# Optimization experiments

Measured on AMD Instinct MI355X. Metric: run time of the kernel, lower is better.

The kernel has to match this reference:

```python
import jax, jax.numpy as jnp
import numpy as np

B, N, D, H_IMG, W_IMG = 1, 6, 128, 28, 60
HB, WB = 50, 50
HEADS, DH = 4, 32
INNER = HEADS * DH  # 128 == D
Q = HB * WB
NK = N * H_IMG * W_IMG


def _ln(x, w, b, eps=1e-5):
    m = jnp.mean(x, axis=-1, keepdims=True)
    v = jnp.var(x, axis=-1, keepdims=True)
    return (x - m) * jax.lax.rsqrt(v + eps) * w + b


def setup_inputs() -> dict:
    key = jax.random.key(0)
    ks = jax.random.split(key, 20)
    s = 0.02
    inp = {
        "q": jax.random.normal(ks[0], (B, D, HB, WB), jnp.float32),
        "k": jax.random.normal(ks[1], (B, N, D, H_IMG, W_IMG), jnp.float32),
        "v": jax.random.normal(ks[2], (B, N, D, H_IMG, W_IMG), jnp.float32),
        "W_logits": jax.random.uniform(ks[3], (B, Q, NK), jnp.float32),
        "vis_flat": jax.random.randint(ks[4], (B, Q, NK), 0, 2).astype(jnp.int32),
        "skip": jax.random.normal(ks[5], (B, D, HB, WB), jnp.float32),
        # LayerNorm params
        "qn_w": jnp.ones((D,), jnp.float32), "qn_b": jnp.zeros((D,), jnp.float32),
        "kn_w": jnp.ones((D,), jnp.float32), "kn_b": jnp.zeros((D,), jnp.float32),
        "vn_w": jnp.ones((D,), jnp.float32), "vn_b": jnp.zeros((D,), jnp.float32),
        "pre_w": jnp.ones((D,), jnp.float32), "pre_b": jnp.zeros((D,), jnp.float32),
        "post_w": jnp.ones((D,), jnp.float32), "post_b": jnp.zeros((D,), jnp.float32),
        # Linear params, stored [in, out]
        "wq": jax.random.normal(ks[6], (D, INNER), jnp.float32) * s,
        "bq": jnp.zeros((INNER,), jnp.float32),
        "wk": jax.random.normal(ks[7], (D, INNER), jnp.float32) * s,
        "bk": jnp.zeros((INNER,), jnp.float32),
        "wv": jax.random.normal(ks[8], (D, INNER), jnp.float32) * s,
        "bv": jnp.zeros((INNER,), jnp.float32),
        "wp": jax.random.normal(ks[9], (INNER, D), jnp.float32) * s,
        "bp": jnp.zeros((D,), jnp.float32),
        "w1": jax.random.normal(ks[10], (D, 2 * D), jnp.float32) * s,
        "b1": jnp.zeros((2 * D,), jnp.float32),
        "w2": jax.random.normal(ks[11], (2 * D, D), jnp.float32) * s,
        "b2": jnp.zeros((D,), jnp.float32),
    }
    return inp


def reference(q, k, v, W_logits, vis_flat, skip,
              qn_w, qn_b, kn_w, kn_b, vn_w, vn_b, pre_w, pre_b, post_w, post_b,
              wq, bq, wk, bk, wv, bv, wp, bp, w1, b1, w2, b2):
    b, d, Hb, Wb = q.shape
    _, n, _, hi, wi = k.shape
    Qn = Hb * Wb
    # b d H W -> b (H W) d ; b n d h w -> b (n h w) d
    qf = q.reshape(b, d, Qn).transpose(0, 2, 1)
    kf = k.transpose(0, 1, 3, 4, 2).reshape(b, n * hi * wi, d)
    vf = v.transpose(0, 1, 3, 4, 2).reshape(b, n * hi * wi, d)
    qf = _ln(qf, qn_w, qn_b)
    kf = _ln(kf, kn_w, kn_b)
    vf = _ln(vf, vn_w, vn_b)
    qh = (qf @ wq + bq).reshape(b, Qn, HEADS, DH).transpose(0, 2, 1, 3)
    kh = (kf @ wk + bk).reshape(b, -1, HEADS, DH).transpose(0, 2, 1, 3)
    vh = (vf @ wv + bv).reshape(b, -1, HEADS, DH).transpose(0, 2, 1, 3)
    scale = DH ** (-0.5)
    logits = jnp.einsum('bhqd,bhkd->bhqk', qh, kh) * scale  # [b,h,Q,NK]
    neg_inf = jnp.finfo(logits.dtype).min
    logits = jnp.where(vis_flat[:, None] == 0, neg_inf, logits)
    logits = logits * W_logits[:, None]  # multiplicative EAF weighting
    attn = jax.nn.softmax(logits, axis=-1)
    out = jnp.einsum('bhqk,bhkd->bhqd', attn, vh)
    out = out.transpose(0, 2, 1, 3).reshape(b, Qn, INNER)
    out = out @ wp + bp
    z = out + skip.reshape(b, d, Qn).transpose(0, 2, 1)
    z = _ln(z, pre_w, pre_b)
    z = z + (jax.nn.gelu(z @ w1 + b1, approximate=False) @ w2 + b2)
    z = _ln(z, post_w, post_b)
    return z.transpose(0, 2, 1).reshape(b, d, Hb, Wb)
```

## Files before the change

### kernel.cpp

```cpp
#include <hip/hip_runtime.h>
#include <hip/hip_bf16.h>
#include <math.h>

typedef short short8 __attribute__((ext_vector_type(8)));
typedef float floatx4 __attribute__((ext_vector_type(4)));
typedef int   intx4  __attribute__((ext_vector_type(4)));

#define D 128
#define Q 2500
#define QPAD 2560
#define NK 10080
#define NKPAD 10112
#define SPLITS 19
#define CPS 17
#define OPS 163904
#define LPS 10304
#define VBW 320
#define VROW 40
#define QSCALE 0.25501268426834347f
#define NEGBIG -3.0e38f

#define LDS_BARRIER() asm volatile("s_waitcnt lgkmcnt(0)\n\ts_barrier" ::: "memory")

__device__ __forceinline__ unsigned short f2bf(float f) {
    unsigned u = __float_as_uint(f);
    unsigned r = (u + 0x7fffu + ((u >> 16) & 1u)) >> 16;
    return (unsigned short)r;
}
__device__ __forceinline__ unsigned pack2bf(float lo, float hi) {
    unsigned u0 = __float_as_uint(lo) + 0x8000u;
    unsigned u1 = __float_as_uint(hi) + 0x8000u;
    return (u0 >> 16) | (u1 & 0xffff0000u);
}
__device__ __forceinline__ unsigned cvtpk(float lo, float hi) {
    unsigned r;
    asm("v_cvt_pk_bf16_f32 %0, %1, %2" : "=v"(r) : "v"(lo), "v"(hi));
    return r;
}
__device__ __forceinline__ float bflo(unsigned u) { return __uint_as_float(u << 16); }
__device__ __forceinline__ float bfhi(unsigned u) { return __uint_as_float(u & 0xffff0000u); }

__global__ __launch_bounds__(256) void prep_kernel(
    const float* __restrict__ qi, const float* __restrict__ ki, const float* __restrict__ vi,
    const float* __restrict__ qw, const float* __restrict__ qb_,
    const float* __restrict__ kw, const float* __restrict__ kb,
    const float* __restrict__ vw, const float* __restrict__ vb,
    unsigned short* __restrict__ xq, unsigned short* __restrict__ xk,
    unsigned short* __restrict__ xv,
    const float* __restrict__ wq, const float* __restrict__ wk,
    const float* __restrict__ wv, const float* __restrict__ wp,
    const float* __restrict__ w1, const float* __restrict__ w2,
    unsigned short* __restrict__ wqT, unsigned short* __restrict__ wkT,
    unsigned short* __restrict__ wvT, unsigned short* __restrict__ wpT,
    unsigned short* __restrict__ w1T, unsigned short* __restrict__ w2T,
    const int* __restrict__ vis, unsigned* __restrict__ vbits) {
    int bid = blockIdx.x, t = threadIdx.x;
    if (bid >= 1227) {
        int row = bid - 1227;
        const int* src = vis + (size_t)row * NK;
        #pragma unroll 2
        for (int w = t; w < 315; w += 256) {
            unsigned bits = 0;
            const intx4* p = (const intx4*)(src + w * 32);
            #pragma unroll
            for (int g = 0; g < 8; g++) {
                intx4 v = p[g];
                #pragma unroll
                for (int j = 0; j < 4; j++) bits |= (v[j] ? 1u : 0u) << (g * 4 + j);
            }
            vbits[(size_t)row * VBW + w] = bits;
        }
        return;
    }
    if (bid >= 715) {
        int idx = (bid - 715) * 256 + t;
        if (idx < 49152) {
            int m = idx >> 14;
            int local = idx & 16383;
            int n = local >> 7, kk = local & 127;
            const float* w = (m == 0) ? wq : ((m == 1) ? wk : wv);
            unsigned short* o = (m == 0) ? wqT : ((m == 1) ? wkT : wvT);
            o[local] = f2bf(w[kk * 128 + n]);
        } else if (idx < 65536) {
            int local = idx - 49152;
            int n = local >> 7, kk = local & 127;
            wpT[local] = f2bf(wp[kk * 128 + n]);
        } else if (idx < 98304) {
            int local = idx - 65536;
            int n = local >> 7, kk = local & 127;
            w1T[local] = f2bf(w1[kk * 256 + n]);
        } else {
            int local = idx - 98304;
            int n = local >> 8, kk = local & 255;
            w2T[local] = f2bf(w2[kk * 128 + n]);
        }
        return;
    }
    __shared__ float lds2[32 * 132];
    const float* src; unsigned short* dst; const float *g, *b;
    int S, valid;
    if (bid < 79) {
        int p0 = bid * 32;
        src = qi + p0; S = Q; dst = xq + p0 * D; g = qw; b = qb_;
        valid = Q - p0; if (valid > 32) valid = 32;
    } else if (bid < 397) {
        int tt = bid - 79;
        int n = tt / 53, tile = tt - n * 53, r = tile * 32;
        src = ki + (size_t)(n * 128) * 1680 + r; S = 1680;
        dst = xk + (n * 1680 + r) * D; g = kw; b = kb;
        valid = 1680 - r; if (valid > 32) valid = 32;
    } else {
        int tt = bid - 397;
        int n = tt / 53, tile = tt - n * 53, r = tile * 32;
        src = vi + (size_t)(n * 128) * 1680 + r; S = 1680;
        dst = xv + (n * 1680 + r) * D; g = vw; b = vb;
        valid = 1680 - r; if (valid > 32) valid = 32;
    }
    #pragma unroll
    for (int pass = 0; pass < 4; pass++) {
        int s = pass * 256 + t;
        int d = s >> 3, ps = s & 7;
        floatx4 val = {0.f, 0.f, 0.f, 0.f};
        if (ps * 4 < valid) val = *(const floatx4*)(src + (size_t)d * S + ps * 4);
        #pragma unroll
        for (int j = 0; j < 4; j++) lds2[(ps * 4 + j) * 132 + d] = val[j];
    }
    __syncthreads();
    int lane = t & 63, wvx = t >> 6;
    int pos = wvx * 8 + (lane >> 3), l7 = lane & 7;
    floatx4 x4[4];
    #pragma unroll
    for (int k = 0; k < 4; k++) x4[k] = *(const floatx4*)(&lds2[pos * 132 + l7 * 16 + k * 4]);
    float s = 0.f, ss = 0.f;
    #pragma unroll
    for (int k = 0; k < 4; k++)
        #pragma unroll
        for (int j = 0; j < 4; j++) { s += x4[k][j]; ss += x4[k][j] * x4[k][j]; }
    #pragma unroll
    for (int m = 1; m <= 4; m <<= 1) { s += __shfl_xor(s, m, 64); ss += __shfl_xor(ss, m, 64); }
    float mean = s * (1.0f / 128.0f);
    float var = ss * (1.0f / 128.0f) - mean * mean;
    float rstd = rsqrtf(var + 1e-5f);
    short8 o1, o2;
    #pragma unroll
    for (int k = 0; k < 4; k++) {
        floatx4 g4 = *(const floatx4*)(g + l7 * 16 + k * 4);
        floatx4 b4 = *(const floatx4*)(b + l7 * 16 + k * 4);
        #pragma unroll
        for (int j = 0; j < 4; j++) {
            float o = (x4[k][j] - mean) * rstd * g4[j] + b4[j];
            if (k < 2) o1[k * 4 + j] = (short)f2bf(o);
            else o2[(k - 2) * 4 + j] = (short)f2bf(o);
        }
    }
    if (pos < valid) {
        *(short8*)(dst + pos * D + l7 * 16) = o1;
        *(short8*)(dst + pos * D + l7 * 16 + 8) = o2;
    }
}

__global__ __launch_bounds__(256) void proj_kernel(
    const unsigned short* __restrict__ xq, const unsigned short* __restrict__ xk,
    const unsigned short* __restrict__ xv,
    const unsigned short* __restrict__ wqT, const unsigned short* __restrict__ wkT,
    const unsigned short* __restrict__ wvT,
    const float* __restrict__ bq, const float* __restrict__ bk, const float* __restrict__ bv,
    unsigned short* __restrict__ qh, unsigned short* __restrict__ kh,
    unsigned short* __restrict__ vhT) {
    __shared__ short vlds[128 * 72];
    int bid = blockIdx.x;
    const unsigned short *src, *wT; const float* bias; int mb, mode; float scale;
    if (bid < 40)       { mode = 0; src = xq; wT = wqT; bias = bq; mb = bid * 64; scale = QSCALE; }
    else if (bid < 198) { mode = 1; src = xk; wT = wkT; bias = bk; mb = (bid - 40) * 64; scale = 1.0f; }
    else                { mode = 2; src = xv; wT = wvT; bias = bv; mb = (bid - 198) * 64; scale = 1.0f; }
    int t = threadIdx.x, wave = t >> 6, lane = t & 63;
    int l15 = lane & 15, quad = lane >> 4;
    int m0 = mb + wave * 16;
    floatx4 acc[8];
    #pragma unroll
    for (int i = 0; i < 8; i++) acc[i] = (floatx4){0.f, 0.f, 0.f, 0.f};
    #pragma unroll
    for (int kf = 0; kf < 4; kf++) {
        short8 A = *(const short8*)(src + (m0 + l15) * D + kf * 32 + quad * 8);
        #pragma unroll
        for (int nt = 0; nt < 8; nt++) {
            short8 Bv = *(const short8*)(wT + (nt * 16 + l15) * D + kf * 32 + quad * 8);
            acc[nt] = __builtin_amdgcn_mfma_f32_16x16x32_bf16(A, Bv, acc[nt], 0, 0, 0);
        }
    }
    if (mode != 2) {
        unsigned short* dst = (mode == 0) ? qh : kh;
        #pragma unroll
        for (int nt = 0; nt < 8; nt++) {
            float bb = bias[nt * 16 + l15];
            #pragma unroll
            for (int r = 0; r < 4; r++)
                dst[(m0 + quad * 4 + r) * D + nt * 16 + l15] = f2bf((acc[nt][r] + bb) * scale);
        }
    } else {
        #pragma unroll
        for (int nt = 0; nt < 8; nt++) {
            float bb = bias[nt * 16 + l15];
            #pragma unroll
            for (int r = 0; r < 4; r++)
                vlds[(nt * 16 + l15) * 72 + (wave * 16 + quad * 4 + r)] =
                    (short)f2bf(acc[nt][r] + bb);
        }
        __syncthreads();
        int pr = t & 31, dd = t >> 5;
        int sub = pr >> 4, i = pr & 15;
        #pragma unroll
        for (int pass = 0; pass < 16; pass++) {
            int d = pass * 8 + dd;
            unsigned lo = (unsigned short)vlds[d * 72 + sub * 32 + i];
            unsigned hi = (unsigned short)vlds[d * 72 + sub * 32 + 16 + i];
            *(unsigned*)(vhT + (size_t)d * NKPAD + mb + sub * 32 + 2 * i) = lo | (hi << 16);
        }
    }
}

template<int USEBITS>
__global__ __launch_bounds__(256, 3) void attn_kernel_t(
    const unsigned short* __restrict__ qh, const unsigned short* __restrict__ kh,
    const unsigned short* __restrict__ vhT,
    const float* __restrict__ Wl, const int* __restrict__ vis,
    const unsigned* __restrict__ vbits,
    unsigned* __restrict__ OpartU, float* __restrict__ lpart) {
    __shared__ short Kl[2][32 * 136];
    __shared__ short Vl[2][128 * VROW];
    int bid = blockIdx.x;
    int split = bid % SPLITS, qt = bid / SPLITS;
    int t = threadIdx.x, wave = t >> 6, lane = t & 63;
    int l15 = lane & 15, quad = lane >> 4;
    int qb = qt * 64 + wave * 16;
    int k00 = split * (CPS * 32);
    int cmax = (NK - k00) >> 5; if (cmax > CPS) cmax = CPS;

    short8 qB[4];
    #pragma unroll
    for (int h = 0; h < 4; h++)
        qB[h] = *(const short8*)(qh + (size_t)(qb + l15) * D + h * 32 + quad * 8);

    int kr = t >> 3, ks = (t & 7) * 2;
    int vd = t >> 1, vs = (t & 1) * 2;
    const uint4* ksrc = (const uint4*)(kh + (size_t)(k00 + kr) * D + ks * 8);
    const uint4* vsrc = (const uint4*)(vhT + (size_t)vd * NKPAD + k00 + vs * 8);
    short* kdst = &Kl[0][kr * 136 + ks * 8];
    short* vdst = &Vl[0][vd * VROW + vs * 8];

    int wrow = qb + l15; if (wrow >= Q) wrow = Q - 1;
    const float* wp = Wl + (size_t)wrow * NK + k00 + quad * 4;
    const int*   vp = vis + (size_t)wrow * NK + k00 + quad * 4;
    const unsigned* vbp = vbits + (size_t)wrow * VBW + split * CPS;

    int idxA = l15 + ((quad & 1) << 5);
    int idxB = idxA + 16;
    bool hiK = (quad >= 2);

    const floatx4 zf = {0.f, 0.f, 0.f, 0.f};
    floatx4 O[4][2];
    float lacc[4];
    #pragma unroll
    for (int h = 0; h < 4; h++) { O[h][0] = zf; O[h][1] = zf; lacc[h] = 0.f; }

    uint4 ka = ksrc[0], kb2 = ksrc[1];
    uint4 va = vsrc[0], vb2 = vsrc[1];
    floatx4 wc0 = *(const floatx4*)wp;
    floatx4 wc1 = *(const floatx4*)(wp + 16);
    floatx4 wn0, wn1;
    intx4 vc0, vc1;
    unsigned vbc = 0, vbn = 0;
    if constexpr (USEBITS) {
        vbc = vbp[0];
        wn0 = *(const floatx4*)(wp + 32);
        wn1 = *(const floatx4*)(wp + 48);
        vbn = vbp[1];
    } else {
        vc0 = *(const intx4*)vp;
        vc1 = *(const intx4*)(vp + 16);
    }
    *(uint4*)kdst = ka;       *(uint4*)(kdst + 8) = kb2;
    *(uint4*)vdst = va;       *(uint4*)(vdst + 8) = vb2;

    #pragma unroll 1
    for (int c = 0; c < cmax; c++) {
        LDS_BARRIER();
        int buf = c & 1;
        uint4 nka, nkb, nva, nvb;
        floatx4 w20, w21; intx4 vn0, vn1;
        unsigned vb2n = 0;
        if (c + 1 < cmax) {
            const uint4* ks2 = ksrc + (size_t)(c + 1) * 512;
            const uint4* vs2 = vsrc + (size_t)(c + 1) * 4;
            nka = ks2[0]; nkb = ks2[1];
            nva = vs2[0]; nvb = vs2[1];
        }
        if constexpr (USEBITS) {
            if (c + 2 < cmax) {
                w20 = *(const floatx4*)(wp + (c + 2) * 32);
                w21 = *(const floatx4*)(wp + (c + 2) * 32 + 16);
                vb2n = vbp[c + 2];
            }
        } else {
            if (c + 1 < cmax) {
                wn0 = *(const floatx4*)(wp + (c + 1) * 32);
                wn1 = *(const floatx4*)(wp + (c + 1) * 32 + 16);
                vn0 = *(const intx4*)(vp + (c + 1) * 32);
                vn1 = *(const intx4*)(vp + (c + 1) * 32 + 16);
            }
        }
        float a2[8], b2[8];
        if constexpr (USEBITS) {
            unsigned bq = vbc >> (quad * 4);
            #pragma unroll
            for (int r = 0; r < 4; r++) {
                bool m0 = (bq >> r) & 1u;
                bool m1 = (bq >> (16 + r)) & 1u;
                a2[r]     = m0 ? wc0[r] : 0.f;
                b2[r]     = m0 ? 0.f : wc0[r] * NEGBIG;
                a2[4 + r] = m1 ? wc1[r] : 0.f;
                b2[4 + r] = m1 ? 0.f : wc1[r] * NEGBIG;
            }
        } else {
            #pragma unroll
            for (int r = 0; r < 4; r++) {
                a2[r]     = vc0[r] ? wc0[r] : 0.f;
                b2[r]     = vc0[r] ? 0.f : wc0[r] * NEGBIG;
                a2[4 + r] = vc1[r] ? wc1[r] : 0.f;
                b2[4 + r] = vc1[r] ? 0.f : wc1[r] * NEGBIG;
            }
        }
        const short* Kb = Kl[buf];
        const short* Vb = Vl[buf];
        __builtin_amdgcn_s_setprio(1);
        #pragma unroll
        for (int h = 0; h < 4; h++) {
            short8 kA0 = *(const short8*)(Kb + l15 * 136 + h * 32 + quad * 8);
            short8 kA1 = *(const short8*)(Kb + (16 + l15) * 136 + h * 32 + quad * 8);
            floatx4 S0 = __builtin_amdgcn_mfma_f32_16x16x32_bf16(kA0, qB[h], zf, 0, 0, 0);
            floatx4 S1 = __builtin_amdgcn_mfma_f32_16x16x32_bf16(kA1, qB[h], zf, 0, 0, 0);
            float p0[4], p1[4];
            #pragma unroll
            for (int r = 0; r < 4; r++) {
                p0[r] = exp2f(S0[r] * a2[r] + b2[r]);
                p1[r] = exp2f(S1[r] * a2[4 + r] + b2[4 + r]);
                lacc[h] += p0[r] + p1[r];
            }
            unsigned u0 = cvtpk(p0[0], p0[1]);
            unsigned u1 = cvtpk(p0[2], p0[3]);
            unsigned u2 = cvtpk(p1[0], p1[1]);
            unsigned u3 = cvtpk(p1[2], p1[3]);
            unsigned s0A = __shfl(u0, idxA, 64), s2A = __shfl(u2, idxA, 64);
            unsigned s1A = __shfl(u1, idxA, 64), s3A = __shfl(u3, idxA, 64);
            unsigned s0B = __shfl(u0, idxB, 64), s2B = __shfl(u2, idxB, 64);
            unsigned s1B = __shfl(u1, idxB, 64), s3B = __shfl(u3, idxB, 64);
            union { unsigned u[4]; short8 s8; } pb;
            pb.u[0] = hiK ? s2A : s0A;
            pb.u[1] = hiK ? s3A : s1A;
            pb.u[2] = hiK ? s2B : s0B;
            pb.u[3] = hiK ? s3B : s1B;
            short8 vA0 = *(const short8*)(Vb + (h * 32 + l15) * VROW + quad * 8);
            short8 vA1 = *(const short8*)(Vb + (h * 32 + 16 + l15) * VROW + quad * 8);
            O[h][0] = __builtin_amdgcn_mfma_f32_16x16x32_bf16(vA0, pb.s8, O[h][0], 0, 0, 0);
            O[h][1] = __builtin_amdgcn_mfma_f32_16x16x32_bf16(vA1, pb.s8, O[h][1], 0, 0, 0);
        }
        __builtin_amdgcn_s_setprio(0);
        if (c + 1 < cmax) {
            short* kd = buf ? kdst : (kdst + 32 * 136);
            short* vd2 = buf ? vdst : (vdst + 128 * VROW);
            *(uint4*)kd = nka;       *(uint4*)(kd + 8) = nkb;
            *(uint4*)vd2 = nva;      *(uint4*)(vd2 + 8) = nvb;
        }
        if constexpr (USEBITS) {
            wc0 = wn0; wc1 = wn1; vbc = vbn;
            if (c + 2 < cmax) { wn0 = w20; wn1 = w21; vbn = vb2n; }
        } else {
            if (c + 1 < cmax) { wc0 = wn0; wc1 = wn1; vc0 = vn0; vc1 = vn1; }
        }
    }

    int row = qb + l15;
    #pragma unroll
    for (int h = 0; h < 4; h++) {
        float lv = lacc[h];
        lv += __shfl_xor(lv, 16, 64);
        lv += __shfl_xor(lv, 32, 64);
        if (quad == 0) lpart[(size_t)split * LPS + row * 4 + h] = lv;
        #pragma unroll
        for (int tl = 0; tl < 2; tl++) {
            uint2 o2;
            o2.x = cvtpk(O[h][tl][0], O[h][tl][1]);
            o2.y = cvtpk(O[h][tl][2], O[h][tl][3]);
            *(uint2*)(OpartU + (size_t)split * OPS + ((size_t)row * 4 + h) * 16 + tl * 8 + quad * 2) = o2;
        }
    }
}

__global__ __launch_bounds__(128) void combine_kernel(
    const unsigned* __restrict__ Opart, const float* __restrict__ lpart,
    unsigned* __restrict__ A1u) {
    int tid = blockIdx.x * 128 + threadIdx.x;
    int sl = tid & 3, he = (tid >> 2) & 3, grow = tid >> 4;
    float lsum = 0.f;
    #pragma unroll 5
    for (int sp = 0; sp < SPLITS; sp++) lsum += lpart[(size_t)sp * LPS + grow * 4 + he];
    float inv = 1.0f / fmaxf(lsum, 1e-30f);
    size_t base = ((size_t)grow * 4 + he) * 16 + sl * 4;
    float a0 = 0.f, a1 = 0.f, a2 = 0.f, a3 = 0.f, a4 = 0.f, a5 = 0.f, a6 = 0.f, a7 = 0.f;
    #pragma unroll 5
    for (int sp = 0; sp < SPLITS; sp++) {
        uint4 u = *(const uint4*)(Opart + (size_t)sp * OPS + base);
        a0 += bflo(u.x); a1 += bfhi(u.x);
        a2 += bflo(u.y); a3 += bfhi(u.y);
        a4 += bflo(u.z); a5 += bfhi(u.z);
        a6 += bflo(u.w); a7 += bfhi(u.w);
    }
    uint4 o;
    o.x = pack2bf(a0 * inv, a1 * inv);
    o.y = pack2bf(a2 * inv, a3 * inv);
    o.z = pack2bf(a4 * inv, a5 * inv);
    o.w = pack2bf(a6 * inv, a7 * inv);
    *(uint4*)(A1u + (size_t)grow * 64 + he * 16 + sl * 4) = o;
}

__global__ __launch_bounds__(256) void mlp_kernel(
    const unsigned short* __restrict__ A1,
    const unsigned short* __restrict__ wpT,
    const float* __restrict__ bp, const float* __restrict__ skip,
    const float* __restrict__ pre_w, const float* __restrict__ pre_b,
    const unsigned short* __restrict__ w1T, const float* __restrict__ b1,
    const unsigned short* __restrict__ w2T, const float* __restrict__ b2,
    const float* __restrict__ post_w, const float* __restrict__ post_b,
    float* __restrict__ out) {
    __shared__ __align__(16) char smem[51200];
    short* Z1 = (short*)smem;
    short* H1 = (short*)(smem + 17408);
    float* Zout = (float*)smem;

    int qb = blockIdx.x * 64;
    int t = threadIdx.x, wave = t >> 6, lane = t & 63;
    int l15 = lane & 15, quad = lane >> 4;
    int m0 = wave * 16;

    floatx4 z[8];
    #pragma unroll
    for (int i = 0; i < 8; i++) z[i] = (floatx4){0.f, 0.f, 0.f, 0.f};
    #pragma unroll
    for (int kf = 0; kf < 4; kf++) {
        short8 A = *(const short8*)(A1 + (size_t)(qb + m0 + l15) * 128 + kf * 32 + quad * 8);
        #pragma unroll
        for (int nt = 0; nt < 8; nt++) {
            short8 Bv = *(const short8*)(wpT + (nt * 16 + l15) * D + kf * 32 + quad * 8);
            z[nt] = __builtin_amdgcn_mfma_f32_16x16x32_bf16(A, Bv, z[nt], 0, 0, 0);
        }
    }
    float Zv[8][4];
    #pragma unroll
    for (int nt = 0; nt < 8; nt++) {
        int n = nt * 16 + l15;
        float bb = bp[n];
        #pragma unroll
        for (int r = 0; r < 4; r++) {
            int q = qb + m0 + quad * 4 + r;
            int qc = q < Q ? q : (Q - 1);
            Zv[nt][r] = z[nt][r] + bb + skip[n * Q + qc];
        }
    }
    float Zn[8][4];
    {
        #pragma unroll
        for (int r = 0; r < 4; r++) {
            float s1 = 0.f, s2 = 0.f;
            #pragma unroll
            for (int nt = 0; nt < 8; nt++) { s1 += Zv[nt][r]; s2 += Zv[nt][r] * Zv[nt][r]; }
            #pragma unroll
            for (int m = 1; m <= 8; m <<= 1) { s1 += __shfl_xor(s1, m, 64); s2 += __shfl_xor(s2, m, 64); }
            float mean = s1 * (1.0f / 128.0f);
            float var = s2 * (1.0f / 128.0f) - mean * mean;
            float rstd = rsqrtf(var + 1e-5f);
            #pragma unroll
            for (int nt = 0; nt < 8; nt++) Zn[nt][r] = (Zv[nt][r] - mean) * rstd;
        }
        #pragma unroll
        for (int nt = 0; nt < 8; nt++) {
            int n = nt * 16 + l15;
            float g = pre_w[n], be = pre_b[n];
            #pragma unroll
            for (int r = 0; r < 4; r++) {
                Zn[nt][r] = Zn[nt][r] * g + be;
                Z1[(m0 + quad * 4 + r) * 136 + n] = (short)f2bf(Zn[nt][r]);
            }
        }
    }
    {
        floatx4 h2[16];
        #pragma unroll
        for (int i = 0; i < 16; i++) h2[i] = (floatx4){0.f, 0.f, 0.f, 0.f};
        #pragma unroll
        for (int kf = 0; kf < 4; kf++) {
            short8 A = *(const short8*)(Z1 + (m0 + l15) * 136 + kf * 32 + quad * 8);
            #pragma unroll
            for (int nt = 0; nt < 16; nt++) {
                short8 Bv = *(const short8*)(w1T + (nt * 16 + l15) * D + kf * 32 + quad * 8);
                h2[nt] = __builtin_amdgcn_mfma_f32_16x16x32_bf16(A, Bv, h2[nt], 0, 0, 0);
            }
        }
        #pragma unroll
        for (int nt = 0; nt < 16; nt++) {
            int n = nt * 16 + l15;
            float bb = b1[n];
            #pragma unroll
            for (int r = 0; r < 4; r++) {
                float x = h2[nt][r] + bb;
                float gl = 0.5f * x * (1.0f + erff(x * 0.70710678118654752f));
                H1[(m0 + quad * 4 + r) * 264 + n] = (short)f2bf(gl);
            }
        }
    }
    floatx4 o3[8];
    #pragma unroll
    for (int i = 0; i < 8; i++) o3[i] = (floatx4){0.f, 0.f, 0.f, 0.f};
    #pragma unroll
    for (int kf = 0; kf < 8; kf++) {
        short8 A = *(const short8*)(H1 + (m0 + l15) * 264 + kf * 32 + quad * 8);
        #pragma unroll
        for (int nt = 0; nt < 8; nt++) {
            short8 Bv = *(const short8*)(w2T + (nt * 16 + l15) * 256 + kf * 32 + quad * 8);
            o3[nt] = __builtin_amdgcn_mfma_f32_16x16x32_bf16(A, Bv, o3[nt], 0, 0, 0);
        }
    }
    float Z2[8][4];
    #pragma unroll
    for (int nt = 0; nt < 8; nt++) {
        int n = nt * 16 + l15;
        float bb = b2[n];
        #pragma unroll
        for (int r = 0; r < 4; r++) Z2[nt][r] = Zn[nt][r] + o3[nt][r] + bb;
    }
    float Zo[8][4];
    {
        #pragma unroll
        for (int r = 0; r < 4; r++) {
            float s1 = 0.f, s2 = 0.f;
            #pragma unroll
            for (int nt = 0; nt < 8; nt++) { s1 += Z2[nt][r]; s2 += Z2[nt][r] * Z2[nt][r]; }
            #pragma unroll
            for (int m = 1; m <= 8; m <<= 1) { s1 += __shfl_xor(s1, m, 64); s2 += __shfl_xor(s2, m, 64); }
            float mean = s1 * (1.0f / 128.0f);
            float var = s2 * (1.0f / 128.0f) - mean * mean;
            float rstd = rsqrtf(var + 1e-5f);
            #pragma unroll
            for (int nt = 0; nt < 8; nt++) Zo[nt][r] = (Z2[nt][r] - mean) * rstd;
        }
        #pragma unroll
        for (int nt = 0; nt < 8; nt++) {
            int n = nt * 16 + l15;
            float g = post_w[n], be = post_b[n];
            #pragma unroll
            for (int r = 0; r < 4; r++) Zo[nt][r] = Zo[nt][r] * g + be;
        }
    }
    __syncthreads();
    #pragma unroll
    for (int nt = 0; nt < 8; nt++)
        #pragma unroll
        for (int r = 0; r < 4; r++)
            Zout[(nt * 16 + l15) * 65 + m0 + quad * 4 + r] = Zo[nt][r];
    __syncthreads();
    {
        int pl = t & 63;
        int q = qb + pl;
        if (q < Q) {
            #pragma unroll
            for (int it = 0; it < 32; it++) {
                int n = it * 4 + (t >> 6);
                out[n * Q + q] = Zout[n * 65 + pl];
            }
        }
    }
}

extern "C" void kernel_launch(void* const* d_in, const int* in_sizes, int n_in,
                              void* d_out, int out_size, void* d_ws, size_t ws_size,
                              hipStream_t stream) {
    (void)in_sizes; (void)n_in; (void)out_size;
    const float* q      = (const float*)d_in[0];
    const float* k      = (const float*)d_in[1];
    const float* v      = (const float*)d_in[2];
    const float* Wl     = (const float*)d_in[3];
    const int*   vis    = (const int*)  d_in[4];
    const float* skip   = (const float*)d_in[5];
    const float* qn_w   = (const float*)d_in[6];
    const float* qn_b   = (const float*)d_in[7];
    const float* kn_w   = (const float*)d_in[8];
    const float* kn_b   = (const float*)d_in[9];
    const float* vn_w   = (const float*)d_in[10];
    const float* vn_b   = (const float*)d_in[11];
    const float* pre_w  = (const float*)d_in[12];
    const float* pre_b  = (const float*)d_in[13];
    const float* post_w = (const float*)d_in[14];
    const float* post_b = (const float*)d_in[15];
    const float* wq     = (const float*)d_in[16];
    const float* bq     = (const float*)d_in[17];
    const float* wk     = (const float*)d_in[18];
    const float* bk     = (const float*)d_in[19];
    const float* wv     = (const float*)d_in[20];
    const float* bv     = (const float*)d_in[21];
    const float* wp     = (const float*)d_in[22];
    const float* bp     = (const float*)d_in[23];
    const float* w1     = (const float*)d_in[24];
    const float* b1     = (const float*)d_in[25];
    const float* w2     = (const float*)d_in[26];
    const float* b2     = (const float*)d_in[27];
    float* out = (float*)d_out;

    char* ws = (char*)d_ws;
    unsigned short* xq  = (unsigned short*)(ws + 0);
    unsigned short* xk  = (unsigned short*)(ws + 655360);
    unsigned short* xv  = (unsigned short*)(ws + 3244032);
    unsigned short* qh  = (unsigned short*)(ws + 5832704);
    unsigned short* kh  = (unsigned short*)(ws + 6488064);
    unsigned short* vhT = (unsigned short*)(ws + 9076736);
    unsigned short* wqT = (unsigned short*)(ws + 11665408);
    unsigned short* wkT = (unsigned short*)(ws + 11698176);
    unsigned short* wvT = (unsigned short*)(ws + 11730944);
    unsigned short* wpT = (unsigned short*)(ws + 11763712);
    unsigned short* w1T = (unsigned short*)(ws + 11796480);
    unsigned short* w2T = (unsigned short*)(ws + 11862016);
    unsigned* OpartU    = (unsigned*)(ws + 11927552);
    float* lpart        = (float*)(ws + 34874112);
    unsigned* vbits     = (unsigned*)(ws + 36316672);
    unsigned* A1u       = (unsigned*)(ws + 0);

    const bool usebits = (ws_size == 0) || (ws_size >= 39520000ull);

    prep_kernel<<<dim3(usebits ? 3727 : 1227), dim3(256), 0, stream>>>(
        q, k, v, qn_w, qn_b, kn_w, kn_b, vn_w, vn_b, xq, xk, xv,
        wq, wk, wv, wp, w1, w2, wqT, wkT, wvT, wpT, w1T, w2T, vis, vbits);
    proj_kernel<<<dim3(356), dim3(256), 0, stream>>>(xq, xk, xv, wqT, wkT, wvT, bq, bk, bv,
                                                     qh, kh, vhT);
    if (usebits)
        attn_kernel_t<1><<<dim3(40 * SPLITS), dim3(256), 0, stream>>>(
            qh, kh, vhT, Wl, vis, vbits, OpartU, lpart);
    else
        attn_kernel_t<0><<<dim3(40 * SPLITS), dim3(256), 0, stream>>>(
            qh, kh, vhT, Wl, vis, vbits, OpartU, lpart);
    combine_kernel<<<dim3(320), dim3(128), 0, stream>>>(OpartU, lpart, A1u);
    mlp_kernel<<<dim3(40), dim3(256), 0, stream>>>((const unsigned short*)A1u, wpT, bp, skip,
                                                   pre_w, pre_b, w1T, b1, w2T, b2,
                                                   post_w, post_b, out);
}
```

Before: 358.5 us.

## Process two 64-row query tiles per attention block to reuse staged K/V tiles

Each attention block now covers 128 query rows instead of 64. Every wave runs two 16-row query sub-tiles against the same K/V chunk in LDS, so each K/V load from global memory and LDS read feeds twice as many MFMAs. To keep the grid large, the key dimension is split into 25 chunks of 13 instead of 19 of 17. The LDS row padding for K and V changes, launch bounds drop to 2 blocks per CU, and the W/visibility prefetch depth for the bitmask path goes from two chunks ahead to one. The cost is higher register pressure and lower occupancy, plus more partial outputs for the combine step to reduce.

```diff
diff --git a/kernel.cpp b/kernel.cpp
--- a/kernel.cpp
+++ b/kernel.cpp
@@ -11,12 +11,13 @@
 #define QPAD 2560
 #define NK 10080
 #define NKPAD 10112
-#define SPLITS 19
-#define CPS 17
+#define SPLITS 25
+#define CPS 13
 #define OPS 163904
 #define LPS 10304
 #define VBW 320
-#define VROW 40
+#define KROW 152
+#define VROW 48
 #define QSCALE 0.25501268426834347f
 #define NEGBIG -3.0e38f
 
@@ -220,64 +221,69 @@
 }
 
 template<int USEBITS>
-__global__ __launch_bounds__(256, 3) void attn_kernel_t(
+__global__ __launch_bounds__(256, 2) void attn_kernel_t(
     const unsigned short* __restrict__ qh, const unsigned short* __restrict__ kh,
     const unsigned short* __restrict__ vhT,
     const float* __restrict__ Wl, const int* __restrict__ vis,
     const unsigned* __restrict__ vbits,
     unsigned* __restrict__ OpartU, float* __restrict__ lpart) {
-    __shared__ short Kl[2][32 * 136];
+    __shared__ short Kl[2][32 * KROW];
     __shared__ short Vl[2][128 * VROW];
     int bid = blockIdx.x;
     int split = bid % SPLITS, qt = bid / SPLITS;
     int t = threadIdx.x, wave = t >> 6, lane = t & 63;
     int l15 = lane & 15, quad = lane >> 4;
-    int qb = qt * 64 + wave * 16;
+    int qb = qt * 128 + wave * 16;
     int k00 = split * (CPS * 32);
     int cmax = (NK - k00) >> 5; if (cmax > CPS) cmax = CPS;
 
-    short8 qB[4];
-    #pragma unroll
-    for (int h = 0; h < 4; h++)
-        qB[h] = *(const short8*)(qh + (size_t)(qb + l15) * D + h * 32 + quad * 8);
+    short8 qB[2][4];
+    #pragma unroll
+    for (int tt = 0; tt < 2; tt++)
+        #pragma unroll
+        for (int h = 0; h < 4; h++)
+            qB[tt][h] = *(const short8*)(qh + (size_t)(qb + tt * 64 + l15) * D + h * 32 + quad * 8);
 
     int kr = t >> 3, ks = (t & 7) * 2;
     int vd = t >> 1, vs = (t & 1) * 2;
     const uint4* ksrc = (const uint4*)(kh + (size_t)(k00 + kr) * D + ks * 8);
     const uint4* vsrc = (const uint4*)(vhT + (size_t)vd * NKPAD + k00 + vs * 8);
-    short* kdst = &Kl[0][kr * 136 + ks * 8];
+    short* kdst = &Kl[0][kr * KROW + ks * 8];
     short* vdst = &Vl[0][vd * VROW + vs * 8];
 
-    int wrow = qb + l15; if (wrow >= Q) wrow = Q - 1;
-    const float* wp = Wl + (size_t)wrow * NK + k00 + quad * 4;
-    const int*   vp = vis + (size_t)wrow * NK + k00 + quad * 4;
-    const unsigned* vbp = vbits + (size_t)wrow * VBW + split * CPS;
+    int wrow0 = qb + l15;      if (wrow0 >= Q) wrow0 = Q - 1;
+    int wrow1 = qb + 64 + l15; if (wrow1 >= Q) wrow1 = Q - 1;
+    const float* wp0 = Wl + (size_t)wrow0 * NK + k00 + quad * 4;
+    const float* wp1 = Wl + (size_t)wrow1 * NK + k00 + quad * 4;
+    const int*   vp0 = vis + (size_t)wrow0 * NK + k00 + quad * 4;
+    const int*   vp1 = vis + (size_t)wrow1 * NK + k00 + quad * 4;
+    const unsigned* vbp0 = vbits + (size_t)wrow0 * VBW + split * CPS;
+    const unsigned* vbp1 = vbits + (size_t)wrow1 * VBW + split * CPS;
 
     int idxA = l15 + ((quad & 1) << 5);
     int idxB = idxA + 16;
     bool hiK = (quad >= 2);
 
     const floatx4 zf = {0.f, 0.f, 0.f, 0.f};
-    floatx4 O[4][2];
-    float lacc[4];
-    #pragma unroll
-    for (int h = 0; h < 4; h++) { O[h][0] = zf; O[h][1] = zf; lacc[h] = 0.f; }
+    floatx4 O[2][4][2];
+    float lacc[2][4];
+    #pragma unroll
+    for (int tt = 0; tt < 2; tt++)
+        #pragma unroll
+        for (int h = 0; h < 4; h++) { O[tt][h][0] = zf; O[tt][h][1] = zf; lacc[tt][h] = 0.f; }
 
     uint4 ka = ksrc[0], kb2 = ksrc[1];
     uint4 va = vsrc[0], vb2 = vsrc[1];
-    floatx4 wc0 = *(const floatx4*)wp;
-    floatx4 wc1 = *(const floatx4*)(wp + 16);
-    floatx4 wn0, wn1;
-    intx4 vc0, vc1;
-    unsigned vbc = 0, vbn = 0;
+    floatx4 wc0[2], wc1[2];
+    intx4 vc0[2], vc1[2];
+    unsigned vbc[2];
+    wc0[0] = *(const floatx4*)wp0;       wc1[0] = *(const floatx4*)(wp0 + 16);
+    wc0[1] = *(const floatx4*)wp1;       wc1[1] = *(const floatx4*)(wp1 + 16);
     if constexpr (USEBITS) {
-        vbc = vbp[0];
-        wn0 = *(const floatx4*)(wp + 32);
-        wn1 = *(const floatx4*)(wp + 48);
-        vbn = vbp[1];
+        vbc[0] = vbp0[0]; vbc[1] = vbp1[0];
     } else {
-        vc0 = *(const intx4*)vp;
-        vc1 = *(const intx4*)(vp + 16);
+        vc0[0] = *(const intx4*)vp0; vc1[0] = *(const intx4*)(vp0 + 16);
+        vc0[1] = *(const intx4*)vp1; vc1[1] = *(const intx4*)(vp1 + 16);
     }
     *(uint4*)kdst = ka;       *(uint4*)(kdst + 8) = kb2;
     *(uint4*)vdst = va;       *(uint4*)(vdst + 8) = vb2;
@@ -287,47 +293,49 @@
         LDS_BARRIER();
         int buf = c & 1;
         uint4 nka, nkb, nva, nvb;
-        floatx4 w20, w21; intx4 vn0, vn1;
-        unsigned vb2n = 0;
+        floatx4 wn0[2], wn1[2];
+        intx4 vn0[2], vn1[2];
+        unsigned vbn[2];
         if (c + 1 < cmax) {
             const uint4* ks2 = ksrc + (size_t)(c + 1) * 512;
             const uint4* vs2 = vsrc + (size_t)(c + 1) * 4;
             nka = ks2[0]; nkb = ks2[1];
             nva = vs2[0]; nvb = vs2[1];
-        }
-        if constexpr (USEBITS) {
-            if (c + 2 < cmax) {
-                w20 = *(const floatx4*)(wp + (c + 2) * 32);
-                w21 = *(const floatx4*)(wp + (c + 2) * 32 + 16);
-                vb2n = vbp[c + 2];
-            }
-        } else {
-            if (c + 1 < cmax) {
-                wn0 = *(const floatx4*)(wp + (c + 1) * 32);
-                wn1 = *(const floatx4*)(wp + (c + 1) * 32 + 16);
-                vn0 = *(const intx4*)(vp + (c + 1) * 32);
-                vn1 = *(const intx4*)(vp + (c + 1) * 32 + 16);
-            }
-        }
-        float a2[8], b2[8];
-        if constexpr (USEBITS) {
-            unsigned bq = vbc >> (quad * 4);
-            #pragma unroll
-            for (int r = 0; r < 4; r++) {
-                bool m0 = (bq >> r) & 1u;
-                bool m1 = (bq >> (16 + r)) & 1u;
-                a2[r]     = m0 ? wc0[r] : 0.f;
-                b2[r]     = m0 ? 0.f : wc0[r] * NEGBIG;
-                a2[4 + r] = m1 ? wc1[r] : 0.f;
-                b2[4 + r] = m1 ? 0.f : wc1[r] * NEGBIG;
-            }
-        } else {
-            #pragma unroll
-            for (int r = 0; r < 4; r++) {
-                a2[r]     = vc0[r] ? wc0[r] : 0.f;
-                b2[r]     = vc0[r] ? 0.f : wc0[r] * NEGBIG;
-                a2[4 + r] = vc1[r] ? wc1[r] : 0.f;
-                b2[4 + r] = vc1[r] ? 0.f : wc1[r] * NEGBIG;
+            wn0[0] = *(const floatx4*)(wp0 + (c + 1) * 32);
+            wn1[0] = *(const floatx4*)(wp0 + (c + 1) * 32 + 16);
+            wn0[1] = *(const floatx4*)(wp1 + (c + 1) * 32);
+            wn1[1] = *(const floatx4*)(wp1 + (c + 1) * 32 + 16);
+            if constexpr (USEBITS) {
+                vbn[0] = vbp0[c + 1]; vbn[1] = vbp1[c + 1];
+            } else {
+                vn0[0] = *(const intx4*)(vp0 + (c + 1) * 32);
+                vn1[0] = *(const intx4*)(vp0 + (c + 1) * 32 + 16);
+                vn0[1] = *(const intx4*)(vp1 + (c + 1) * 32);
+                vn1[1] = *(const intx4*)(vp1 + (c + 1) * 32 + 16);
+            }
+        }
+        float a2[2][8], b2[2][8];
+        #pragma unroll
+        for (int tt = 0; tt < 2; tt++) {
+            if constexpr (USEBITS) {
+                unsigned bq = vbc[tt] >> (quad * 4);
+                #pragma unroll
+                for (int r = 0; r < 4; r++) {
+                    bool m0 = (bq >> r) & 1u;
+                    bool m1 = (bq >> (16 + r)) & 1u;
+                    a2[tt][r]     = m0 ? wc0[tt][r] : 0.f;
+                    b2[tt][r]     = m0 ? 0.f : wc0[tt][r] * NEGBIG;
+                    a2[tt][4 + r] = m1 ? wc1[tt][r] : 0.f;
+                    b2[tt][4 + r] = m1 ? 0.f : wc1[tt][r] * NEGBIG;
+                }
+            } else {
+                #pragma unroll
+                for (int r = 0; r < 4; r++) {
+                    a2[tt][r]     = vc0[tt][r] ? wc0[tt][r] : 0.f;
+                    b2[tt][r]     = vc0[tt][r] ? 0.f : wc0[tt][r] * NEGBIG;
+                    a2[tt][4 + r] = vc1[tt][r] ? wc1[tt][r] : 0.f;
+                    b2[tt][4 + r] = vc1[tt][r] ? 0.f : wc1[tt][r] * NEGBIG;
+                }
             }
         }
         const short* Kb = Kl[buf];
@@ -335,63 +343,69 @@
         __builtin_amdgcn_s_setprio(1);
         #pragma unroll
         for (int h = 0; h < 4; h++) {
-            short8 kA0 = *(const short8*)(Kb + l15 * 136 + h * 32 + quad * 8);
-            short8 kA1 = *(const short8*)(Kb + (16 + l15) * 136 + h * 32 + quad * 8);
-            floatx4 S0 = __builtin_amdgcn_mfma_f32_16x16x32_bf16(kA0, qB[h], zf, 0, 0, 0);
-            floatx4 S1 = __builtin_amdgcn_mfma_f32_16x16x32_bf16(kA1, qB[h], zf, 0, 0, 0);
-            float p0[4], p1[4];
-            #pragma unroll
-            for (int r = 0; r < 4; r++) {
-                p0[r] = exp2f(S0[r] * a2[r] + b2[r]);
-                p1[r] = exp2f(S1[r] * a2[4 + r] + b2[4 + r]);
-                lacc[h] += p0[r] + p1[r];
-            }
-            unsigned u0 = cvtpk(p0[0], p0[1]);
-            unsigned u1 = cvtpk(p0[2], p0[3]);
-            unsigned u2 = cvtpk(p1[0], p1[1]);
-            unsigned u3 = cvtpk(p1[2], p1[3]);
-            unsigned s0A = __shfl(u0, idxA, 64), s2A = __shfl(u2, idxA, 64);
-            unsigned s1A = __shfl(u1, idxA, 64), s3A = __shfl(u3, idxA, 64);
-            unsigned s0B = __shfl(u0, idxB, 64), s2B = __shfl(u2, idxB, 64);
-            unsigned s1B = __shfl(u1, idxB, 64), s3B = __shfl(u3, idxB, 64);
-            union { unsigned u[4]; short8 s8; } pb;
-            pb.u[0] = hiK ? s2A : s0A;
-            pb.u[1] = hiK ? s3A : s1A;
-            pb.u[2] = hiK ? s2B : s0B;
-            pb.u[3] = hiK ? s3B : s1B;
+            short8 kA0 = *(const short8*)(Kb + l15 * KROW + h * 32 + quad * 8);
+            short8 kA1 = *(const short8*)(Kb + (16 + l15) * KROW + h * 32 + quad * 8);
             short8 vA0 = *(const short8*)(Vb + (h * 32 + l15) * VROW + quad * 8);
             short8 vA1 = *(const short8*)(Vb + (h * 32 + 16 + l15) * VROW + quad * 8);
-            O[h][0] = __builtin_amdgcn_mfma_f32_16x16x32_bf16(vA0, pb.s8, O[h][0], 0, 0, 0);
-            O[h][1] = __builtin_amdgcn_mfma_f32_16x16x32_bf16(vA1, pb.s8, O[h][1], 0, 0, 0);
+            #pragma unroll
+            for (int tt = 0; tt < 2; tt++) {
+                floatx4 S0 = __builtin_amdgcn_mfma_f32_16x16x32_bf16(kA0, qB[tt][h], zf, 0, 0, 0);
+                floatx4 S1 = __builtin_amdgcn_mfma_f32_16x16x32_bf16(kA1, qB[tt][h], zf, 0, 0, 0);
+                float p0[4], p1[4];
+                #pragma unroll
+                for (int r = 0; r < 4; r++) {
+                    p0[r] = exp2f(S0[r] * a2[tt][r] + b2[tt][r]);
+                    p1[r] = exp2f(S1[r] * a2[tt][4 + r] + b2[tt][4 + r]);
+                    lacc[tt][h] += p0[r] + p1[r];
+                }
+                unsigned u0 = cvtpk(p0[0], p0[1]);
+                unsigned u1 = cvtpk(p0[2], p0[3]);
+                unsigned u2 = cvtpk(p1[0], p1[1]);
+                unsigned u3 = cvtpk(p1[2], p1[3]);
+                unsigned s0A = __shfl(u0, idxA, 64), s2A = __shfl(u2, idxA, 64);
+                unsigned s1A = __shfl(u1, idxA, 64), s3A = __shfl(u3, idxA, 64);
+                unsigned s0B = __shfl(u0, idxB, 64), s2B = __shfl(u2, idxB, 64);
+                unsigned s1B = __shfl(u1, idxB, 64), s3B = __shfl(u3, idxB, 64);
+                union { unsigned u[4]; short8 s8; } pb;
+                pb.u[0] = hiK ? s2A : s0A;
+                pb.u[1] = hiK ? s3A : s1A;
+                pb.u[2] = hiK ? s2B : s0B;
+                pb.u[3] = hiK ? s3B : s1B;
+                O[tt][h][0] = __builtin_amdgcn_mfma_f32_16x16x32_bf16(vA0, pb.s8, O[tt][h][0], 0, 0, 0);
+                O[tt][h][1] = __builtin_amdgcn_mfma_f32_16x16x32_bf16(vA1, pb.s8, O[tt][h][1], 0, 0, 0);
+            }
         }
         __builtin_amdgcn_s_setprio(0);
         if (c + 1 < cmax) {
-            short* kd = buf ? kdst : (kdst + 32 * 136);
+            short* kd = buf ? kdst : (kdst + 32 * KROW);
             short* vd2 = buf ? vdst : (vdst + 128 * VROW);
             *(uint4*)kd = nka;       *(uint4*)(kd + 8) = nkb;
             *(uint4*)vd2 = nva;      *(uint4*)(vd2 + 8) = nvb;
-        }
-        if constexpr (USEBITS) {
-            wc0 = wn0; wc1 = wn1; vbc = vbn;
-            if (c + 2 < cmax) { wn0 = w20; wn1 = w21; vbn = vb2n; }
-        } else {
-            if (c + 1 < cmax) { wc0 = wn0; wc1 = wn1; vc0 = vn0; vc1 = vn1; }
-        }
-    }
-
-    int row = qb + l15;
-    #pragma unroll
-    for (int h = 0; h < 4; h++) {
-        float lv = lacc[h];
-        lv += __shfl_xor(lv, 16, 64);
-        lv += __shfl_xor(lv, 32, 64);
-        if (quad == 0) lpart[(size_t)split * LPS + row * 4 + h] = lv;
-        #pragma unroll
-        for (int tl = 0; tl < 2; tl++) {
-            uint2 o2;
-            o2.x = cvtpk(O[h][tl][0], O[h][tl][1]);
-            o2.y = cvtpk(O[h][tl][2], O[h][tl][3]);
-            *(uint2*)(OpartU + (size_t)split * OPS + ((size_t)row * 4 + h) * 16 + tl * 8 + quad * 2) = o2;
+            #pragma unroll
+            for (int tt = 0; tt < 2; tt++) {
+                wc0[tt] = wn0[tt]; wc1[tt] = wn1[tt];
+                if constexpr (USEBITS) { vbc[tt] = vbn[tt]; }
+                else { vc0[tt] = vn0[tt]; vc1[tt] = vn1[tt]; }
+            }
+        }
+    }
+
+    #pragma unroll
+    for (int tt = 0; tt < 2; tt++) {
+        int row = qb + tt * 64 + l15;
+        #pragma unroll
+        for (int h = 0; h < 4; h++) {
+            float lv = lacc[tt][h];
+            lv += __shfl_xor(lv, 16, 64);
+            lv += __shfl_xor(lv, 32, 64);
+            if (quad == 0) lpart[(size_t)split * LPS + row * 4 + h] = lv;
+            #pragma unroll
+            for (int tl = 0; tl < 2; tl++) {
+                uint2 o2;
+                o2.x = cvtpk(O[tt][h][tl][0], O[tt][h][tl][1]);
+                o2.y = cvtpk(O[tt][h][tl][2], O[tt][h][tl][3]);
+                *(uint2*)(OpartU + (size_t)split * OPS + ((size_t)row * 4 + h) * 16 + tl * 8 + quad * 2) = o2;
+            }
         }
     }
 }
@@ -640,10 +654,10 @@
     proj_kernel<<<dim3(356), dim3(256), 0, stream>>>(xq, xk, xv, wqT, wkT, wvT, bq, bk, bv,
                                                      qh, kh, vhT);
     if (usebits)
-        attn_kernel_t<1><<<dim3(40 * SPLITS), dim3(256), 0, stream>>>(
+        attn_kernel_t<1><<<dim3(20 * SPLITS), dim3(256), 0, stream>>>(
             qh, kh, vhT, Wl, vis, vbits, OpartU, lpart);
     else
-        attn_kernel_t<0><<<dim3(40 * SPLITS), dim3(256), 0, stream>>>(
+        attn_kernel_t<0><<<dim3(20 * SPLITS), dim3(256), 0, stream>>>(
             qh, kh, vhT, Wl, vis, vbits, OpartU, lpart);
     combine_kernel<<<dim3(320), dim3(128), 0, stream>>>(OpartU, lpart, A1u);
     mlp_kernel<<<dim3(40), dim3(256), 0, stream>>>((const unsigned short*)A1u, wpT, bp, skip,
```

Measured after the change: 434.1 us. 21.1% more time.
